# Kernel tuning notes

Measured on AMD Instinct MI355X. Metric: run time of the kernel, lower is better.

The kernel has to match this reference:

```python
import jax, jax.numpy as jnp
import numpy as np

N_USERS = 100000
N_ITEMS = 50000
N_NODES = N_USERS + N_ITEMS
N_INTER = 3200000
DIM = 64
N_LAYERS = 3


def setup_inputs() -> dict:
    key = jax.random.key(0)
    k1, k2, k3, k4, k5, k6 = jax.random.split(key, 6)
    # Embedding tables, init N(0, 0.1) as in nn.init.normal_(std=0.1)
    user_emb = 0.1 * jax.random.normal(k1, (N_USERS, DIM), dtype=jnp.float32)
    item_emb = 0.1 * jax.random.normal(k2, (N_ITEMS, DIM), dtype=jnp.float32)
    # Random bipartite interactions, symmetrized
    u = jax.random.randint(k3, (N_INTER,), 0, N_USERS, dtype=jnp.int32)
    i = jax.random.randint(k4, (N_INTER,), 0, N_ITEMS, dtype=jnp.int32) + N_USERS
    edge_src = jnp.concatenate([u, i])  # [2*N_INTER]
    edge_dst = jnp.concatenate([i, u])
    # Symmetric normalization D^-1/2 A D^-1/2 (as in getSparseGraph)
    deg = jax.ops.segment_sum(jnp.ones_like(edge_src, dtype=jnp.float32), edge_src,
                              num_segments=N_NODES)
    d_inv_sqrt = jnp.where(deg > 0, 1.0 / jnp.sqrt(deg), 0.0)
    edge_val = d_inv_sqrt[edge_src] * d_inv_sqrt[edge_dst]
    users = jax.random.randint(k5, (4096,), 0, N_USERS, dtype=jnp.int32)
    items = jax.random.randint(k6, (4096,), 0, N_ITEMS, dtype=jnp.int32)
    return {"user_emb": user_emb, "item_emb": item_emb,
            "edge_src": edge_src, "edge_dst": edge_dst, "edge_val": edge_val,
            "users": users, "items": items}


def _spmm(edge_src, edge_dst, edge_val, x):
    # y[r] = sum_{e: src[e]=r} val[e] * x[dst[e]]
    return jax.ops.segment_sum(edge_val[:, None] * x[edge_dst], edge_src,
                               num_segments=N_NODES)


def reference(user_emb, item_emb, edge_src, edge_dst, edge_val, users, items):
    all_emb = jnp.concatenate([user_emb, item_emb], axis=0)  # [N_NODES, D]
    acc = all_emb
    emb = all_emb
    for _ in range(N_LAYERS):
        emb = _spmm(edge_src, edge_dst, edge_val, emb)
        acc = acc + emb
    light_out = acc / jnp.asarray(N_LAYERS + 1, dtype=all_emb.dtype)
    all_users = light_out[:N_USERS]
    all_items = light_out[N_USERS:]
    u = all_users[users]  # [B, D]
    v = all_items[items]  # [B, D]
    gamma = jnp.sum(u * v, axis=1)  # [B]
    return gamma
```

## Files before the change

kernel.cpp:

```cpp
#include <hip/hip_runtime.h>

#define N_USERS 100000
#define N_ITEMS 50000
#define N_NODES 150000
#define DIM 64
#define NQ 4096
#define GROUP 1024
#define NG ((N_NODES + GROUP - 1) / GROUP)
#define NBLK_A 512
#define NT (NG * NBLK_A)
#define NSB2 ((NT + 1023) / 1024)

typedef __attribute__((ext_vector_type(4))) _Float16 h4;
typedef __attribute__((ext_vector_type(8))) _Float16 h8;

static inline size_t align256(size_t x) { return (x + 255) & ~(size_t)255; }

__global__ void k_count(const int* __restrict__ src, int* __restrict__ T,
                        int nE, int epb) {
    __shared__ int h[NG];
    int tid = threadIdx.x, b = blockIdx.x;
    for (int i = tid; i < NG; i += 256) h[i] = 0;
    __syncthreads();
    int e0 = b * epb, e1 = min(e0 + epb, nE);
    for (int rb = e0; rb < e1; rb += 1024) {
        int e = rb + tid * 4;
        if (e + 3 < e1) {
            int4 s4 = *(const int4*)(src + e);
            atomicAdd(&h[s4.x >> 10], 1);
            atomicAdd(&h[s4.y >> 10], 1);
            atomicAdd(&h[s4.z >> 10], 1);
            atomicAdd(&h[s4.w >> 10], 1);
        } else {
            for (int j = 0; j < 4; ++j) {
                int ee = e + j;
                if (ee < e1) atomicAdd(&h[src[ee] >> 10], 1);
            }
        }
    }
    __syncthreads();
    for (int i = tid; i < NG; i += 256) T[i * NBLK_A + b] = h[i];
}

__global__ void k_scan1(int* __restrict__ T, int* __restrict__ btot) {
    __shared__ int ws[4];
    int blk = blockIdx.x, tid = threadIdx.x;
    int lane = tid & 63, wid = tid >> 6;
    int idx = blk * 1024 + tid * 4;
    int a0 = 0, a1 = 0, a2 = 0, a3 = 0;
    if (idx + 3 < NT) {
        int4 v = *(const int4*)(T + idx);
        a0 = v.x; a1 = v.y; a2 = v.z; a3 = v.w;
    } else {
        if (idx     < NT) a0 = T[idx];
        if (idx + 1 < NT) a1 = T[idx + 1];
        if (idx + 2 < NT) a2 = T[idx + 2];
        if (idx + 3 < NT) a3 = T[idx + 3];
    }
    int s = a0 + a1 + a2 + a3;
    int x = s;
#pragma unroll
    for (int off = 1; off < 64; off <<= 1) {
        int t = __shfl_up(x, off);
        if (lane >= off) x += t;
    }
    if (lane == 63) ws[wid] = x;
    __syncthreads();
    int woff = 0;
    for (int w = 0; w < wid; ++w) woff += ws[w];
    int excl = woff + x - s;
    if (idx + 3 < NT) {
        int4 o; o.x = excl; o.y = excl + a0; o.z = excl + a0 + a1; o.w = excl + a0 + a1 + a2;
        *(int4*)(T + idx) = o;
    } else {
        if (idx     < NT) T[idx]     = excl;
        if (idx + 1 < NT) T[idx + 1] = excl + a0;
        if (idx + 2 < NT) T[idx + 2] = excl + a0 + a1;
        if (idx + 3 < NT) T[idx + 3] = excl + a0 + a1 + a2;
    }
    if (tid == 255) btot[blk] = woff + x;
}

__global__ void k_scan2(int* __restrict__ btot) {
    __shared__ int ws[4];
    int tid = threadIdx.x, lane = tid & 63, wid = tid >> 6;
    int v = (tid < NSB2) ? btot[tid] : 0;
    int x = v;
#pragma unroll
    for (int off = 1; off < 64; off <<= 1) {
        int t = __shfl_up(x, off);
        if (lane >= off) x += t;
    }
    if (lane == 63) ws[wid] = x;
    __syncthreads();
    int woff = 0;
    for (int w = 0; w < wid; ++w) woff += ws[w];
    if (tid < NSB2) btot[tid] = woff + x - v;
}

__global__ void k_scan3(int* __restrict__ T, const int* __restrict__ btot) {
    int blk = blockIdx.x, tid = threadIdx.x;
    int idx = blk * 1024 + tid * 4;
    int add = btot[blk];
    if (idx + 3 < NT) {
        int4 v = *(int4*)(T + idx);
        v.x += add; v.y += add; v.z += add; v.w += add;
        *(int4*)(T + idx) = v;
    } else {
        if (idx     < NT) T[idx]     += add;
        if (idx + 1 < NT) T[idx + 1] += add;
        if (idx + 2 < NT) T[idx + 2] += add;
    }
}

__global__ void k_scatterb(const int* __restrict__ src, const int* __restrict__ dst,
                           const int* __restrict__ T, unsigned int* __restrict__ brec,
                           int nE, int epb) {
    __shared__ int base_[NG];
    __shared__ int cur[NG];
    int tid = threadIdx.x, b = blockIdx.x;
    for (int i = tid; i < NG; i += 256) { base_[i] = T[i * NBLK_A + b]; cur[i] = 0; }
    __syncthreads();
    int e0 = b * epb, e1 = min(e0 + epb, nE);
    for (int rb = e0; rb < e1; rb += 1024) {
        int e = rb + tid * 4;
        if (e + 3 < e1) {
            int4 s4 = *(const int4*)(src + e);
            int4 d4 = *(const int4*)(dst + e);
#pragma unroll
            for (int j = 0; j < 4; ++j) {
                int s = (j == 0) ? s4.x : (j == 1) ? s4.y : (j == 2) ? s4.z : s4.w;
                int d = (j == 0) ? d4.x : (j == 1) ? d4.y : (j == 2) ? d4.z : d4.w;
                int g = s >> 10;
                int c = atomicAdd(&cur[g], 1);
                brec[base_[g] + c] = ((unsigned int)(s & 1023) << 18) | (unsigned int)d;
            }
        } else {
            for (int j = 0; j < 4; ++j) {
                int ee = e + j;
                if (ee < e1) {
                    int s = src[ee];
                    int d = dst[ee];
                    int g = s >> 10;
                    int c = atomicAdd(&cur[g], 1);
                    brec[base_[g] + c] = ((unsigned int)(s & 1023) << 18) | (unsigned int)d;
                }
            }
        }
    }
}

__global__ void k_place(const int* __restrict__ T, const unsigned int* __restrict__ brec,
                        const float* __restrict__ ue, const float* __restrict__ ie,
                        int* __restrict__ rowp, float* __restrict__ dis,
                        float* __restrict__ dis2, float* __restrict__ rdis,
                        int* __restrict__ cdst, h4* __restrict__ w0, int nE) {
    __shared__ int cnt[GROUP];
    __shared__ float sdis[GROUP];
    __shared__ int ws[16];
    int g   = blockIdx.x;
    int nlo = g * GROUP;
    int gn  = min(GROUP, N_NODES - nlo);
    int tid = threadIdx.x;
    int lane = tid & 63, wid = tid >> 6;
    cnt[tid] = 0;
    __syncthreads();
    int beg  = T[g * NBLK_A];
    int endr = (g == NG - 1) ? nE : T[(g + 1) * NBLK_A];
    for (int i = beg + tid; i < endr; i += blockDim.x)
        atomicAdd(&cnt[brec[i] >> 18], 1);
    __syncthreads();
    int mycnt = cnt[tid];
    int x = mycnt;
#pragma unroll
    for (int off = 1; off < 64; off <<= 1) {
        int t = __shfl_up(x, off);
        if (lane >= off) x += t;
    }
    if (lane == 63) ws[wid] = x;
    __syncthreads();
    if (wid == 0 && lane < 16) {
        int s = ws[lane];
        int y = s;
#pragma unroll
        for (int off = 1; off < 16; off <<= 1) {
            int t = __shfl_up(y, off);
            if (lane >= off) y += t;
        }
        ws[lane] = y - s;
    }
    __syncthreads();
    int excl = ws[wid] + x - mycnt;
    float dv = 0.0f;
    if (mycnt > 0) dv = 1.0f / sqrtf((float)mycnt);
    sdis[tid] = dv;
    if (tid < gn) {
        rowp[nlo + tid] = beg + excl;
        float c = (float)mycnt;
        dis [nlo + tid] = dv;
        dis2[nlo + tid] = (mycnt > 0) ? 1.0f / c : 0.0f;
        rdis[nlo + tid] = (mycnt > 0) ? sqrtf(c) : 0.0f;
    }
    if (g == NG - 1 && tid == 0) rowp[N_NODES] = nE;
    cnt[tid] = beg + excl;
    __syncthreads();
    for (int i = beg + tid; i < endr; i += blockDim.x) {
        unsigned int rec = brec[i];
        int s = (int)(rec >> 18);
        int d = (int)(rec & 0x3FFFFu);
        int pos = atomicAdd(&cnt[s], 1);
        cdst[pos] = d;
    }
    for (int r0 = 0; r0 < gn; r0 += 64) {
        int rl = r0 + (tid >> 4);
        if (rl < gn) {
            int node = nlo + rl;
            int kk = tid & 15;
            float4 v = (node < N_USERS)
                ? ((const float4*)ue)[(size_t)node * 16 + kk]
                : ((const float4*)ie)[(size_t)(node - N_USERS) * 16 + kk];
            float s = sdis[rl];
            h4 o;
            o.x = (_Float16)(v.x * s); o.y = (_Float16)(v.y * s);
            o.z = (_Float16)(v.z * s); o.w = (_Float16)(v.w * s);
            w0[(size_t)node * 16 + kk] = o;
        }
    }
}

__global__ void k_spmm_w(const int* __restrict__ rowp, const int* __restrict__ cdst,
                         const float* __restrict__ dis2, const h8* __restrict__ x8,
                         h8* __restrict__ y8) {
    int gw   = (blockIdx.x * blockDim.x + threadIdx.x) >> 6;
    int lane = threadIdx.x & 63;
    if (gw >= N_NODES) return;
    int beg = rowp[gw], end = rowp[gw + 1];
    int g8 = lane >> 3;
    int k  = lane & 7;
    float acc[8] = {0.f, 0.f, 0.f, 0.f, 0.f, 0.f, 0.f, 0.f};
    int len = end - beg;
    int n32 = len & ~31;
    int p = beg;
    for (; p < beg + n32; p += 32) {
        int e0 = p + g8, e1 = e0 + 8, e2 = e0 + 16, e3 = e0 + 24;
        int d0 = cdst[e0], d1 = cdst[e1], d2 = cdst[e2], d3 = cdst[e3];
        h8 a = x8[(size_t)d0 * 8 + k];
        h8 b = x8[(size_t)d1 * 8 + k];
        h8 c = x8[(size_t)d2 * 8 + k];
        h8 d = x8[(size_t)d3 * 8 + k];
#pragma unroll
        for (int j = 0; j < 8; ++j)
            acc[j] += ((float)a[j] + (float)b[j]) + ((float)c[j] + (float)d[j]);
    }
    for (; p + g8 < end; p += 8) {
        int d = cdst[p + g8];
        h8 a = x8[(size_t)d * 8 + k];
#pragma unroll
        for (int j = 0; j < 8; ++j)
            acc[j] += (float)a[j];
    }
#pragma unroll
    for (int off = 8; off < 64; off <<= 1) {
#pragma unroll
        for (int j = 0; j < 8; ++j)
            acc[j] += __shfl_xor(acc[j], off);
    }
    if (lane < 8) {
        float s = dis2[gw];
        h8 o;
#pragma unroll
        for (int j = 0; j < 8; ++j) o[j] = (_Float16)(acc[j] * s);
        y8[(size_t)gw * 8 + lane] = o;
    }
}

__global__ void k_gather_w1(const int* __restrict__ users, const int* __restrict__ items,
                            const float* __restrict__ ue, const float* __restrict__ ie,
                            const float* __restrict__ rdis, const h4* __restrict__ w1,
                            float* __restrict__ acc) {
    int t = blockIdx.x * blockDim.x + threadIdx.x;
    int r = t >> 4;
    int k = t & 15;
    if (r >= 2 * NQ) return;
    int node = (r < NQ) ? users[r] : (N_USERS + items[r - NQ]);
    float4 v = (node < N_USERS)
        ? ((const float4*)ue)[(size_t)node * 16 + k]
        : ((const float4*)ie)[(size_t)(node - N_USERS) * 16 + k];
    h4 wv = w1[(size_t)node * 16 + k];
    float s = rdis[node];
    float4 c;
    c.x = v.x + s * (float)wv.x; c.y = v.y + s * (float)wv.y;
    c.z = v.z + s * (float)wv.z; c.w = v.w + s * (float)wv.w;
    ((float4*)acc)[(size_t)r * 16 + k] = c;
}

__global__ void k_tail(const int* __restrict__ users, const int* __restrict__ items,
                       const int* __restrict__ rowp, const int* __restrict__ cdst,
                       const float* __restrict__ dis, const float* __restrict__ rdis,
                       const h8* __restrict__ x8, const float* __restrict__ acc,
                       float* __restrict__ out) {
    __shared__ float buf[2][64];
    int b = blockIdx.x;
    int w = threadIdx.x >> 6;
    int lane = threadIdx.x & 63;
    int r = b + w * NQ;
    int node = (w == 0) ? users[b] : (N_USERS + items[b]);
    int beg = rowp[node], end = rowp[node + 1];
    int g8 = lane >> 3;
    int k  = lane & 7;
    float s[8] = {0.f, 0.f, 0.f, 0.f, 0.f, 0.f, 0.f, 0.f};
    int len = end - beg;
    int n32 = len & ~31;
    int p = beg;
    for (; p < beg + n32; p += 32) {
        int e0 = p + g8, e1 = e0 + 8, e2 = e0 + 16, e3 = e0 + 24;
        int d0 = cdst[e0], d1 = cdst[e1], d2 = cdst[e2], d3 = cdst[e3];
        h8 a = x8[(size_t)d0 * 8 + k];
        h8 bb = x8[(size_t)d1 * 8 + k];
        h8 c = x8[(size_t)d2 * 8 + k];
        h8 d = x8[(size_t)d3 * 8 + k];
#pragma unroll
        for (int j = 0; j < 8; ++j)
            s[j] += ((float)a[j] + (float)bb[j]) + ((float)c[j] + (float)d[j]);
    }
    for (; p + g8 < end; p += 8) {
        int d = cdst[p + g8];
        h8 a = x8[(size_t)d * 8 + k];
#pragma unroll
        for (int j = 0; j < 8; ++j)
            s[j] += (float)a[j];
    }
#pragma unroll
    for (int off = 8; off < 64; off <<= 1) {
#pragma unroll
        for (int j = 0; j < 8; ++j)
            s[j] += __shfl_xor(s[j], off);
    }
    if (lane < 8) {
        float dn = dis[node], rn = rdis[node];
        h8 wr = x8[(size_t)node * 8 + lane];
        const float* ap = acc + (size_t)r * DIM + lane * 8;
#pragma unroll
        for (int j = 0; j < 8; ++j)
            buf[w][lane * 8 + j] = ap[j] + rn * (float)wr[j] + dn * s[j];
    }
    __syncthreads();
    if (w == 0) {
        float pd = buf[0][lane] * buf[1][lane];
#pragma unroll
        for (int off = 1; off < 64; off <<= 1) pd += __shfl_xor(pd, off);
        if (lane == 0) out[b] = pd * (1.0f / 16.0f);
    }
}

__global__ void k_spmm_atomic(const int* __restrict__ src, const int* __restrict__ dst,
                              const float* __restrict__ val, const float* __restrict__ x,
                              float* __restrict__ y, int nE) {
    int t = blockIdx.x * blockDim.x + threadIdx.x;
    int e = t >> 4;
    int k = t & 15;
    if (e >= nE) return;
    int   s = src[e];
    int   d = dst[e];
    float v = val[e];
    float4 xv = ((const float4*)x)[(size_t)d * 16 + k];
    float* yp = y + (size_t)s * DIM + k * 4;
    atomicAdd(yp + 0, v * xv.x);
    atomicAdd(yp + 1, v * xv.y);
    atomicAdd(yp + 2, v * xv.z);
    atomicAdd(yp + 3, v * xv.w);
}

__global__ void k_concat(const float* __restrict__ ue, const float* __restrict__ ie,
                         float* __restrict__ emb) {
    int i = blockIdx.x * blockDim.x + threadIdx.x;
    const int totalU = N_USERS * DIM / 4;
    const int total  = N_NODES * DIM / 4;
    if (i >= total) return;
    float4 v = (i < totalU) ? ((const float4*)ue)[i] : ((const float4*)ie)[i - totalU];
    ((float4*)emb)[i] = v;
}

__global__ void k_gather(const int* __restrict__ users, const int* __restrict__ items,
                         const float* __restrict__ emb, float* __restrict__ acc,
                         int init) {
    int t = blockIdx.x * blockDim.x + threadIdx.x;
    int r = t >> 4;
    int k = t & 15;
    if (r >= 2 * NQ) return;
    int node = (r < NQ) ? users[r] : (N_USERS + items[r - NQ]);
    float4 v = ((const float4*)emb)[(size_t)node * 16 + k];
    float4* a = ((float4*)acc) + (size_t)r * 16 + k;
    if (init) {
        *a = v;
    } else {
        float4 c = *a;
        c.x += v.x; c.y += v.y; c.z += v.z; c.w += v.w;
        *a = c;
    }
}

__global__ void k_dot(const float* __restrict__ acc, float* __restrict__ out) {
    int i = blockIdx.x * blockDim.x + threadIdx.x;
    if (i >= NQ) return;
    const float* u = acc + (size_t)i * DIM;
    const float* v = acc + (size_t)(NQ + i) * DIM;
    float s = 0.f;
#pragma unroll
    for (int d = 0; d < DIM; ++d) s += u[d] * v[d];
    out[i] = s * (1.0f / 16.0f);
}

extern "C" void kernel_launch(void* const* d_in, const int* in_sizes, int n_in,
                              void* d_out, int out_size, void* d_ws, size_t ws_size,
                              hipStream_t stream) {
    const float* ue    = (const float*)d_in[0];
    const float* ie    = (const float*)d_in[1];
    const int*   esrc  = (const int*)d_in[2];
    const int*   edst  = (const int*)d_in[3];
    const float* ev    = (const float*)d_in[4];
    const int*   users = (const int*)d_in[5];
    const int*   items = (const int*)d_in[6];
    float* out = (float*)d_out;
    const int nE = in_sizes[2];

    const size_t embHB = (size_t)N_NODES * DIM * sizeof(_Float16);
    const size_t accB  = (size_t)2 * NQ * DIM * sizeof(float);
    const size_t rpB   = (size_t)(N_NODES + 1) * sizeof(int);
    const size_t disB  = (size_t)N_NODES * sizeof(float);
    const size_t tB    = (size_t)NT * sizeof(int);
    const size_t btB   = (size_t)NSB2 * sizeof(int);
    const size_t cdB   = (size_t)nE * sizeof(int);

    size_t o = 0;
    char* base = (char*)d_ws;
    h4*    w0    = (h4*)   (base + o); o = align256(o + embHB);
    h4*    w1    = (h4*)   (base + o); o = align256(o + embHB);
    float* acc   = (float*)(base + o); o = align256(o + accB);
    int*   rowp  = (int*)  (base + o); o = align256(o + rpB);
    float* dis   = (float*)(base + o); o = align256(o + disB);
    float* dis2  = (float*)(base + o); o = align256(o + disB);
    float* rdis  = (float*)(base + o); o = align256(o + disB);
    int*   T     = (int*)  (base + o); o = align256(o + tB);
    int*   btot  = (int*)  (base + o); o = align256(o + btB);
    int*   cdst  = (int*)  (base + o); o = align256(o + cdB);
    unsigned int* brec = (unsigned int*)(base + o); o = align256(o + cdB);
    const bool csr_ok = (o <= ws_size);

    if (csr_ok) {
        int epb = ((nE + NBLK_A - 1) / NBLK_A + 3) & ~3;

        k_count<<<NBLK_A, 256, 0, stream>>>(esrc, T, nE, epb);
        k_scan1<<<NSB2, 256, 0, stream>>>(T, btot);
        k_scan2<<<1, 256, 0, stream>>>(btot);
        k_scan3<<<NSB2, 256, 0, stream>>>(T, btot);
        k_scatterb<<<NBLK_A, 256, 0, stream>>>(esrc, edst, T, brec, nE, epb);
        k_place<<<NG, 1024, 0, stream>>>(T, brec, ue, ie, rowp, dis, dis2, rdis,
                                         cdst, w0, nE);

        const int spmmBlocks = (N_NODES * 64 + 255) / 256;
        k_spmm_w<<<spmmBlocks, 256, 0, stream>>>(rowp, cdst, dis2, (const h8*)w0, (h8*)w1);
        k_gather_w1<<<(2 * NQ * 16 + 255) / 256, 256, 0, stream>>>(users, items, ue, ie,
                                                                   rdis, w1, acc);
        k_spmm_w<<<spmmBlocks, 256, 0, stream>>>(rowp, cdst, dis2, (const h8*)w1, (h8*)w0);
        k_tail<<<NQ, 128, 0, stream>>>(users, items, rowp, cdst, dis, rdis,
                                       (const h8*)w0, acc, out);
    } else {
        const size_t embB = (size_t)N_NODES * DIM * sizeof(float);
        size_t o2 = 0;
        float* emb0 = (float*)(base + o2); o2 = align256(o2 + embB);
        float* emb1 = (float*)(base + o2); o2 = align256(o2 + embB);
        float* acc2 = (float*)(base + o2); o2 = align256(o2 + accB);
        const int totalV4 = N_NODES * DIM / 4;
        k_concat<<<(totalV4 + 255) / 256, 256, 0, stream>>>(ue, ie, emb0);
        k_gather<<<(2 * NQ * 16 + 255) / 256, 256, 0, stream>>>(users, items, emb0, acc2, 1);
        float* cur = emb0;
        float* nxt = emb1;
        for (int l = 0; l < 3; ++l) {
            hipMemsetAsync(nxt, 0, embB, stream);
            long threads = (long)nE * 16;
            k_spmm_atomic<<<(int)((threads + 255) / 256), 256, 0, stream>>>(esrc, edst, ev, cur, nxt, nE);
            k_gather<<<(2 * NQ * 16 + 255) / 256, 256, 0, stream>>>(users, items, nxt, acc2, 0);
            float* tmp = cur; cur = nxt; nxt = tmp;
        }
        k_dot<<<(NQ + 255) / 256, 256, 0, stream>>>(acc2, out);
    }
}
```

Measured before the change: 339.2 us.

## Halve CSR bucket size and split embedding scaling into separate kernel

Shrinks the per-block node group from 1024 to 512, doubling the number of place blocks (about 147 to 293) so more CUs are busy during CSR construction. The fp16 scaled-embedding write is moved out of k_place into a new fully parallel k_concat_w kernel. The brec loops in k_place are unrolled four-wide to expose more memory-level parallelism. The trade-off is an extra kernel launch, a second pass over the embedding data, and a prefix-sum table T that doubles in size, which makes the scan kernels do more work.

```diff
diff --git a/kernel.cpp b/kernel.cpp
--- a/kernel.cpp
+++ b/kernel.cpp
@@ -5,7 +5,8 @@
 #define N_NODES 150000
 #define DIM 64
 #define NQ 4096
-#define GROUP 1024
+#define GROUP 512
+#define GSH 9
 #define NG ((N_NODES + GROUP - 1) / GROUP)
 #define NBLK_A 512
 #define NT (NG * NBLK_A)
@@ -15,6 +16,20 @@
 typedef __attribute__((ext_vector_type(8))) _Float16 h8;
 
 static inline size_t align256(size_t x) { return (x + 255) & ~(size_t)255; }
+
+__global__ void k_concat_w(const float* __restrict__ ue, const float* __restrict__ ie,
+                           const float* __restrict__ dis, h4* __restrict__ w) {
+    int i = blockIdx.x * blockDim.x + threadIdx.x;
+    const int totalU = N_USERS * 16;
+    const int total  = N_NODES * 16;
+    if (i >= total) return;
+    float4 v = (i < totalU) ? ((const float4*)ue)[i] : ((const float4*)ie)[i - totalU];
+    float s = dis[i >> 4];
+    h4 o;
+    o.x = (_Float16)(v.x * s); o.y = (_Float16)(v.y * s);
+    o.z = (_Float16)(v.z * s); o.w = (_Float16)(v.w * s);
+    w[i] = o;
+}
 
 __global__ void k_count(const int* __restrict__ src, int* __restrict__ T,
                         int nE, int epb) {
@@ -27,14 +42,14 @@
         int e = rb + tid * 4;
         if (e + 3 < e1) {
             int4 s4 = *(const int4*)(src + e);
-            atomicAdd(&h[s4.x >> 10], 1);
-            atomicAdd(&h[s4.y >> 10], 1);
-            atomicAdd(&h[s4.z >> 10], 1);
-            atomicAdd(&h[s4.w >> 10], 1);
+            atomicAdd(&h[s4.x >> GSH], 1);
+            atomicAdd(&h[s4.y >> GSH], 1);
+            atomicAdd(&h[s4.z >> GSH], 1);
+            atomicAdd(&h[s4.w >> GSH], 1);
         } else {
             for (int j = 0; j < 4; ++j) {
                 int ee = e + j;
-                if (ee < e1) atomicAdd(&h[src[ee] >> 10], 1);
+                if (ee < e1) atomicAdd(&h[src[ee] >> GSH], 1);
             }
         }
     }
@@ -131,9 +146,9 @@
             for (int j = 0; j < 4; ++j) {
                 int s = (j == 0) ? s4.x : (j == 1) ? s4.y : (j == 2) ? s4.z : s4.w;
                 int d = (j == 0) ? d4.x : (j == 1) ? d4.y : (j == 2) ? d4.z : d4.w;
-                int g = s >> 10;
+                int g = s >> GSH;
                 int c = atomicAdd(&cur[g], 1);
-                brec[base_[g] + c] = ((unsigned int)(s & 1023) << 18) | (unsigned int)d;
+                brec[base_[g] + c] = ((unsigned int)(s & (GROUP - 1)) << 18) | (unsigned int)d;
             }
         } else {
             for (int j = 0; j < 4; ++j) {
@@ -141,9 +156,9 @@
                 if (ee < e1) {
                     int s = src[ee];
                     int d = dst[ee];
-                    int g = s >> 10;
+                    int g = s >> GSH;
                     int c = atomicAdd(&cur[g], 1);
-                    brec[base_[g] + c] = ((unsigned int)(s & 1023) << 18) | (unsigned int)d;
+                    brec[base_[g] + c] = ((unsigned int)(s & (GROUP - 1)) << 18) | (unsigned int)d;
                 }
             }
         }
@@ -151,24 +166,33 @@
 }
 
 __global__ void k_place(const int* __restrict__ T, const unsigned int* __restrict__ brec,
-                        const float* __restrict__ ue, const float* __restrict__ ie,
                         int* __restrict__ rowp, float* __restrict__ dis,
                         float* __restrict__ dis2, float* __restrict__ rdis,
-                        int* __restrict__ cdst, h4* __restrict__ w0, int nE) {
+                        int* __restrict__ cdst, int nE) {
     __shared__ int cnt[GROUP];
-    __shared__ float sdis[GROUP];
-    __shared__ int ws[16];
+    __shared__ int ws[8];
     int g   = blockIdx.x;
     int nlo = g * GROUP;
     int gn  = min(GROUP, N_NODES - nlo);
     int tid = threadIdx.x;
     int lane = tid & 63, wid = tid >> 6;
+    const int bs = GROUP;
     cnt[tid] = 0;
     __syncthreads();
     int beg  = T[g * NBLK_A];
     int endr = (g == NG - 1) ? nE : T[(g + 1) * NBLK_A];
-    for (int i = beg + tid; i < endr; i += blockDim.x)
-        atomicAdd(&cnt[brec[i] >> 18], 1);
+    {
+        int i = beg + tid;
+        for (; i + 3 * bs < endr; i += 4 * bs) {
+            unsigned int r0 = brec[i], r1 = brec[i + bs];
+            unsigned int r2 = brec[i + 2 * bs], r3 = brec[i + 3 * bs];
+            atomicAdd(&cnt[r0 >> 18], 1);
+            atomicAdd(&cnt[r1 >> 18], 1);
+            atomicAdd(&cnt[r2 >> 18], 1);
+            atomicAdd(&cnt[r3 >> 18], 1);
+        }
+        for (; i < endr; i += bs) atomicAdd(&cnt[brec[i] >> 18], 1);
+    }
     __syncthreads();
     int mycnt = cnt[tid];
     int x = mycnt;
@@ -179,11 +203,11 @@
     }
     if (lane == 63) ws[wid] = x;
     __syncthreads();
-    if (wid == 0 && lane < 16) {
+    if (wid == 0 && lane < 8) {
         int s = ws[lane];
         int y = s;
 #pragma unroll
-        for (int off = 1; off < 16; off <<= 1) {
+        for (int off = 1; off < 8; off <<= 1) {
             int t = __shfl_up(y, off);
             if (lane >= off) y += t;
         }
@@ -191,39 +215,34 @@
     }
     __syncthreads();
     int excl = ws[wid] + x - mycnt;
-    float dv = 0.0f;
-    if (mycnt > 0) dv = 1.0f / sqrtf((float)mycnt);
-    sdis[tid] = dv;
     if (tid < gn) {
         rowp[nlo + tid] = beg + excl;
         float c = (float)mycnt;
-        dis [nlo + tid] = dv;
-        dis2[nlo + tid] = (mycnt > 0) ? 1.0f / c : 0.0f;
-        rdis[nlo + tid] = (mycnt > 0) ? sqrtf(c) : 0.0f;
+        dis [nlo + tid] = (mycnt > 0) ? 1.0f / sqrtf(c) : 0.0f;
+        dis2[nlo + tid] = (mycnt > 0) ? 1.0f / c        : 0.0f;
+        rdis[nlo + tid] = (mycnt > 0) ? sqrtf(c)        : 0.0f;
     }
     if (g == NG - 1 && tid == 0) rowp[N_NODES] = nE;
     cnt[tid] = beg + excl;
     __syncthreads();
-    for (int i = beg + tid; i < endr; i += blockDim.x) {
-        unsigned int rec = brec[i];
-        int s = (int)(rec >> 18);
-        int d = (int)(rec & 0x3FFFFu);
-        int pos = atomicAdd(&cnt[s], 1);
-        cdst[pos] = d;
-    }
-    for (int r0 = 0; r0 < gn; r0 += 64) {
-        int rl = r0 + (tid >> 4);
-        if (rl < gn) {
-            int node = nlo + rl;
-            int kk = tid & 15;
-            float4 v = (node < N_USERS)
-                ? ((const float4*)ue)[(size_t)node * 16 + kk]
-                : ((const float4*)ie)[(size_t)(node - N_USERS) * 16 + kk];
-            float s = sdis[rl];
-            h4 o;
-            o.x = (_Float16)(v.x * s); o.y = (_Float16)(v.y * s);
-            o.z = (_Float16)(v.z * s); o.w = (_Float16)(v.w * s);
-            w0[(size_t)node * 16 + kk] = o;
+    {
+        int i = beg + tid;
+        for (; i + 3 * bs < endr; i += 4 * bs) {
+            unsigned int r0 = brec[i], r1 = brec[i + bs];
+            unsigned int r2 = brec[i + 2 * bs], r3 = brec[i + 3 * bs];
+            int p0 = atomicAdd(&cnt[r0 >> 18], 1);
+            int p1 = atomicAdd(&cnt[r1 >> 18], 1);
+            int p2 = atomicAdd(&cnt[r2 >> 18], 1);
+            int p3 = atomicAdd(&cnt[r3 >> 18], 1);
+            cdst[p0] = (int)(r0 & 0x3FFFFu);
+            cdst[p1] = (int)(r1 & 0x3FFFFu);
+            cdst[p2] = (int)(r2 & 0x3FFFFu);
+            cdst[p3] = (int)(r3 & 0x3FFFFu);
+        }
+        for (; i < endr; i += bs) {
+            unsigned int rec = brec[i];
+            int pos = atomicAdd(&cnt[rec >> 18], 1);
+            cdst[pos] = (int)(rec & 0x3FFFFu);
         }
     }
 }
@@ -455,9 +474,10 @@
         k_scan2<<<1, 256, 0, stream>>>(btot);
         k_scan3<<<NSB2, 256, 0, stream>>>(T, btot);
         k_scatterb<<<NBLK_A, 256, 0, stream>>>(esrc, edst, T, brec, nE, epb);
-        k_place<<<NG, 1024, 0, stream>>>(T, brec, ue, ie, rowp, dis, dis2, rdis,
-                                         cdst, w0, nE);
-
+        k_place<<<NG, GROUP, 0, stream>>>(T, brec, rowp, dis, dis2, rdis, cdst, nE);
+
+        const int totalH4 = N_NODES * 16;
+        k_concat_w<<<(totalH4 + 255) / 256, 256, 0, stream>>>(ue, ie, dis, w0);
         const int spmmBlocks = (N_NODES * 64 + 255) / 256;
         k_spmm_w<<<spmmBlocks, 256, 0, stream>>>(rowp, cdst, dis2, (const h8*)w0, (h8*)w1);
         k_gather_w1<<<(2 * NQ * 16 + 255) / 256, 256, 0, stream>>>(users, items, ue, ie,
```

Result: faster. 312.2 us (-8.0%).
